# Kernel tuning notes

Measured on AMD Instinct MI355X. Metric: run time of the kernel, lower is better.

## Reference

```python
import jax, jax.numpy as jnp
import numpy as np

DIM = 768
NUM_HEADS = 12
HEAD_DIM = DIM // NUM_HEADS
SCALE = HEAD_DIM ** -0.5


def setup_inputs() -> dict:
    key = jax.random.key(0)
    ks = jax.random.split(key, 9)
    B, L, C = 4, 1024, DIM
    x = jax.random.normal(ks[0], (B, L, C), jnp.float32)
    q_ape = jax.random.normal(ks[1], (1, L, C), jnp.float32)
    k_ape = jax.random.normal(ks[2], (1, L, C), jnp.float32)
    attn_pos = jax.random.normal(ks[3], (1, NUM_HEADS, L, L), jnp.float32)
    s = C ** -0.5
    # torch Linear weights: (out_features, in_features)
    Wq = jax.random.normal(ks[4], (C, C), jnp.float32) * s
    Wk = jax.random.normal(ks[5], (C, C), jnp.float32) * s
    Wv = jax.random.normal(ks[6], (C, C), jnp.float32) * s
    Wp = jax.random.normal(ks[7], (C, C), jnp.float32) * s
    bp = jax.random.normal(ks[8], (C,), jnp.float32) * 0.01
    return {"x": x, "q_ape": q_ape, "k_ape": k_ape, "attn_pos": attn_pos,
            "Wq": Wq, "Wk": Wk, "Wv": Wv, "Wp": Wp, "bp": bp}


def _split_heads(t):
    # (B, L, C) -> (B, H, L, D)
    B, L, C = t.shape
    return t.reshape(B, L, NUM_HEADS, HEAD_DIM).transpose(0, 2, 1, 3)


def reference(x, q_ape, k_ape, attn_pos, Wq, Wk, Wv, Wp, bp):
    B, L, C = x.shape
    q = _split_heads((x + q_ape) @ Wq.T)          # (B,H,L,D)
    k = _split_heads((x + k_ape) @ Wk.T)          # (B,H,L,D)
    v = _split_heads(x @ Wv.T)                    # (B,H,L,D)
    attn = jnp.einsum('bhqd,bhkd->bhqk', q, k) * SCALE + attn_pos
    attn = jax.nn.softmax(attn, axis=-1)
    out = jnp.einsum('bhqk,bhkd->bhqd', attn, v)  # (B,H,L,D)
    out = out.transpose(0, 2, 1, 3).reshape(B, L, C)
    return out @ Wp.T + bp
```

## Files before the change

kernel.cpp:

```cpp
#include <hip/hip_runtime.h>
#include <stdint.h>

#define NH 12
#define HD 64
#define NB 4
#define SEQ 1024
#define CDIM 768
#define MTOT (NB*SEQ)
#define MC   (MTOT*CDIM)
#define LC   (SEQ*CDIM)
#define WSZ  (CDIM*CDIM)
#define LST  104
#define EST  136
#define VST  72
#define L2E  1.44269504f
#define BHSZ (SEQ*HD)

typedef __attribute__((ext_vector_type(4))) float f32x4;
typedef __attribute__((ext_vector_type(8))) __bf16 bf16x8;
typedef __attribute__((ext_vector_type(8))) short short8;
typedef __attribute__((ext_vector_type(4))) unsigned short ushort4v;
typedef unsigned short u16;

static __device__ __forceinline__ f32x4 mfma16(short8 a, short8 b, f32x4 c) {
  return __builtin_amdgcn_mfma_f32_16x16x32_bf16(
      __builtin_bit_cast(bf16x8, a), __builtin_bit_cast(bf16x8, b), c, 0, 0, 0);
}
static __device__ __forceinline__ u16 f2bf(float f) {
  unsigned u = __float_as_uint(f);
  u += 0x7FFFu + ((u >> 16) & 1u);
  return (u16)(u >> 16);
}
static __device__ __forceinline__ float bf2f(u16 h) {
  return __uint_as_float(((unsigned)h) << 16);
}
static __device__ __forceinline__ void lds_load16(const void* g, void* l) {
  __builtin_amdgcn_global_load_lds(
      (const __attribute__((address_space(1))) void*)g,
      (__attribute__((address_space(3))) void*)l, 16, 0, 0);
}

#define PREP_BLKS (MC / 4 / 256)
#define CONV_N4   ((4 * WSZ + CDIM) / 4)
#define CONV_BLKS ((CONV_N4 + 255) / 256)
__global__ __launch_bounds__(256) void prep_all(
    const float* __restrict__ xp, const float* __restrict__ qp,
    const float* __restrict__ kp, const float* __restrict__ Wq,
    const float* __restrict__ Wk, const float* __restrict__ Wv,
    const float* __restrict__ Wp, const float* __restrict__ bp,
    u16* __restrict__ Xq, u16* __restrict__ Xk, u16* __restrict__ Xv,
    u16* __restrict__ Wb) {
  int bid = blockIdx.x;
  if (bid < PREP_BLKS) {
    int i4 = bid * 256 + threadIdx.x;
    int a4 = i4 % (LC / 4);
    f32x4 xx = ((const f32x4*)xp)[i4];
    f32x4 qq = ((const f32x4*)qp)[a4];
    f32x4 kk = ((const f32x4*)kp)[a4];
    ushort4v oq, ok, ov;
#pragma unroll
    for (int j = 0; j < 4; j++) {
      oq[j] = f2bf(xx[j] + qq[j]);
      ok[j] = f2bf(xx[j] + kk[j]);
      ov[j] = f2bf(xx[j]);
    }
    ((ushort4v*)Xq)[i4] = oq;
    ((ushort4v*)Xk)[i4] = ok;
    ((ushort4v*)Xv)[i4] = ov;
  } else {
    int i4 = (bid - PREP_BLKS) * 256 + threadIdx.x;
    if (i4 >= CONV_N4) return;
    int sel = i4 / (WSZ / 4);
    int off = i4 - sel * (WSZ / 4);
    const float* src = sel == 0 ? Wq : sel == 1 ? Wk : sel == 2 ? Wv
                     : sel == 3 ? Wp : bp;
    f32x4 v = ((const f32x4*)src)[off];
    ushort4v o;
#pragma unroll
    for (int j = 0; j < 4; j++) o[j] = f2bf(v[j]);
    ((ushort4v*)Wb)[i4] = o;
  }
}

static __device__ __forceinline__ void gemm_core64(
    const u16* __restrict__ Ab, const u16* __restrict__ Wb,
    short* As, short* Bs, f32x4 acc[2][4]) {
  const int t = threadIdx.x;
  const int lane = t & 63, w = t >> 6, quad = lane >> 4, l16 = lane & 15;
  const int wm = (w >> 1) * 32, wn = (w & 1) * 64;
  const int row4 = t >> 2, chunk = (t & 3) * 8;
  for (int k0 = 0; k0 < CDIM; k0 += 64) {
#pragma unroll
    for (int hh = 0; hh < 2; hh++) {
      const u16* ga = Ab + row4 * CDIM + k0 + hh * 32 + chunk;
      const u16* gb = Wb + row4 * CDIM + k0 + hh * 32 + chunk;
      lds_load16(ga,             (char*)As + hh * 4096 + t * 16);
      lds_load16(gb,             (char*)Bs + hh * 8192 + t * 16);
      lds_load16(gb + 64 * CDIM, (char*)Bs + hh * 8192 + 4096 + t * 16);
    }
    __syncthreads();
#pragma unroll
    for (int hh = 0; hh < 2; hh++) {
      const short* Ah = As + hh * 2048;
      const short* Bh = Bs + hh * 4096;
      short8 af[2], bw[4];
#pragma unroll
      for (int i = 0; i < 2; i++)
        af[i] = *(const short8*)(Ah + (wm + i * 16 + l16) * 32 + quad * 8);
#pragma unroll
      for (int j = 0; j < 4; j++)
        bw[j] = *(const short8*)(Bh + (wn + j * 16 + l16) * 32 + quad * 8);
#pragma unroll
      for (int i = 0; i < 2; i++)
#pragma unroll
        for (int j = 0; j < 4; j++)
          acc[i][j] = mfma16(af[i], bw[j], acc[i][j]);
    }
    __syncthreads();
  }
}

__global__ __launch_bounds__(256) void gemm_qkv(
    const u16* __restrict__ Xq, const u16* __restrict__ Xk, const u16* __restrict__ Xv,
    const u16* __restrict__ Wq, const u16* __restrict__ Wk, const u16* __restrict__ Wv,
    u16* __restrict__ Q, u16* __restrict__ K, u16* __restrict__ Vt) {
  __shared__ __align__(16) short S[12288];
  short* As = S;
  short* Bs = S + 4096;
  const int z = blockIdx.z;
  const int m0 = blockIdx.y * 64, n0 = blockIdx.x * 128;
  const u16* A = (z == 0 ? Xq : z == 1 ? Xk : Xv) + m0 * CDIM;
  const u16* W = (z == 0 ? Wq : z == 1 ? Wk : Wv) + n0 * CDIM;
  f32x4 acc[2][4];
#pragma unroll
  for (int i = 0; i < 2; i++)
#pragma unroll
    for (int j = 0; j < 4; j++) acc[i][j] = 0.f;
  gemm_core64(A, W, As, Bs, acc);

  const int t = threadIdx.x, lane = t & 63, w = t >> 6;
  const int quad = lane >> 4, l16 = lane & 15;
  const int wm = (w >> 1) * 32, wn = (w & 1) * 64;
  const float qs = (z == 0) ? 0.125f : 1.0f;

#pragma unroll
  for (int i = 0; i < 2; i++)
#pragma unroll
    for (int j = 0; j < 4; j++)
#pragma unroll
      for (int r = 0; r < 4; r++) {
        int mr = wm + i * 16 + quad * 4 + r;
        int nc = wn + j * 16 + l16;
        if (z < 2) S[mr * EST + nc] = (short)f2bf(acc[i][j][r] * qs);
        else       S[nc * VST + mr] = (short)f2bf(acc[i][j][r]);
      }
  __syncthreads();

  const int row = t >> 3, ch = t & 7;
  const int b = m0 >> 10, lbase = m0 & 1023;
  if (z == 0) {
#pragma unroll
    for (int cp = 0; cp < 2; cp++) {
      int h = (n0 >> 6) + cp;
#pragma unroll
      for (int rp = 0; rp < 2; rp++) {
        int mr = row + rp * 32;
        short8 v = *(const short8*)(S + mr * EST + cp * 64 + ch * 8);
        *(short8*)(Q + ((((size_t)(b * NH + h)) << 10) + lbase + mr) * HD + ch * 8) = v;
      }
    }
  } else if (z == 1) {
#pragma unroll
    for (int cp = 0; cp < 2; cp++) {
      int h = (n0 >> 6) + cp;
      u16* Kp = K + (size_t)(b * NH + h) * BHSZ;
#pragma unroll
      for (int rp = 0; rp < 2; rp++) {
        int mr = row + rp * 32;
        int tok = lbase + mr;
        short8 v = *(const short8*)(S + mr * EST + cp * 64 + ch * 8);
        *(short8*)(Kp + (((tok >> 4) * 8 + ch) * 16 + (tok & 15)) * 8) = v;
      }
    }
  } else {
#pragma unroll
    for (int rp = 0; rp < 4; rp++) {
      int rn = row + rp * 32;
      int h = (n0 + rn) >> 6, d = rn & 63;
      u16* Vp = Vt + (size_t)(b * NH + h) * BHSZ;
      int jv = d >> 4, ld16 = d & 15;
      int tok = lbase + ch * 8;
      short8 v = *(const short8*)(S + rn * VST + ch * 8);
      *(short8*)(Vp + ((((tok >> 6) * 4 + jv) * 8 + ((tok >> 3) & 7)) * 16 + ld16) * 8) = v;
    }
  }
}

__global__ __launch_bounds__(256, 3) void attn(
    const u16* __restrict__ Q, const u16* __restrict__ Kf, const u16* __restrict__ Vf,
    const float* __restrict__ pos, u16* __restrict__ O) {
  __shared__ __align__(16) short Ps[4 * 16 * LST];
  const int t = threadIdx.x, lane = t & 63, w = t >> 6;
  const int quad = lane >> 4, l16 = lane & 15;

  const int lid = blockIdx.x;
  const int k8 = lid & 7, m = lid >> 3;
  const int g = k8 * 24 + (m >> 2), b = m & 3;
  const int h = g >> 4, qt = g & 15;
  const int bh = b * NH + h;
  const int q0 = qt * 64 + w * 16;

  const u16* Kg = Kf + (size_t)bh * BHSZ;
  const u16* Vg = Vf + (size_t)bh * BHSZ;
  const float* Pg = pos + (size_t)(h * SEQ + q0) * SEQ;
  short* Pw = Ps + w * 16 * LST;
  const int fo = quad * 128 + l16 * 8;

  const u16* Qg = Q + ((size_t)bh * SEQ + q0) * HD;
  const short8 qa0 = *(const short8*)(Qg + l16 * HD + quad * 8);
  const short8 qa1 = *(const short8*)(Qg + l16 * HD + 32 + quad * 8);

  f32x4 o[4];
  float lrow[4];
#pragma unroll
  for (int j = 0; j < 4; j++) o[j] = 0.f;
#pragma unroll
  for (int r = 0; r < 4; r++) lrow[r] = 0.f;

  short8 kb0[4], kb1[4];
  float pf[16];
#pragma unroll
  for (int j = 0; j < 4; j++) {
    kb0[j] = *(const short8*)(Kg + j * 1024 + fo);
    kb1[j] = *(const short8*)(Kg + j * 1024 + 512 + fo);
  }
#pragma unroll
  for (int j = 0; j < 4; j++)
#pragma unroll
    for (int r = 0; r < 4; r++)
      pf[j * 4 + r] = Pg[(quad * 4 + r) * SEQ + j * 16 + l16] * L2E;

#pragma unroll 1
  for (int kt = 0; kt < 16; ++kt) {
    const int kbase = kt * 4096;
    short8 vb0[4], vb1[4];
#pragma unroll
    for (int j = 0; j < 4; j++) {
      vb0[j] = *(const short8*)(Vg + kbase + j * 1024 + fo);
      vb1[j] = *(const short8*)(Vg + kbase + j * 1024 + 512 + fo);
    }
    f32x4 s[4];
#pragma unroll
    for (int j = 0; j < 4; j++) {
      f32x4 zz = 0.f;
      s[j] = mfma16(qa1, kb1[j], mfma16(qa0, kb0[j], zz));
    }
#pragma unroll
    for (int j = 0; j < 4; j++)
#pragma unroll
      for (int r = 0; r < 4; r++) {
        float e = __builtin_amdgcn_exp2f(fmaf(s[j][r], L2E, pf[j * 4 + r]));
        unsigned bits = __float_as_uint(e);
        Pw[(quad * 4 + r) * LST + j * 16 + l16] = (short)(bits >> 16);
        lrow[r] += __uint_as_float(bits & 0xFFFF0000u);
      }
    if (kt < 15) {
      const int nb = kbase + 4096;
#pragma unroll
      for (int j = 0; j < 4; j++) {
        kb0[j] = *(const short8*)(Kg + nb + j * 1024 + fo);
        kb1[j] = *(const short8*)(Kg + nb + j * 1024 + 512 + fo);
      }
      const float* pg = Pg + (kt + 1) * 64;
#pragma unroll
      for (int j = 0; j < 4; j++)
#pragma unroll
        for (int r = 0; r < 4; r++)
          pf[j * 4 + r] = pg[(quad * 4 + r) * SEQ + j * 16 + l16] * L2E;
    }
    const short8 pa0 = *(const short8*)(Pw + l16 * LST + quad * 8);
    const short8 pa1 = *(const short8*)(Pw + l16 * LST + 32 + quad * 8);
#pragma unroll
    for (int j = 0; j < 4; j++)
      o[j] = mfma16(pa1, vb1[j], mfma16(pa0, vb0[j], o[j]));
  }

#pragma unroll
  for (int off = 1; off < 16; off <<= 1)
#pragma unroll
    for (int r = 0; r < 4; r++) lrow[r] += __shfl_xor(lrow[r], off);

  u16* Og = O + ((size_t)b * SEQ + q0) * CDIM + h * HD;
  float inv[4];
#pragma unroll
  for (int r = 0; r < 4; r++) inv[r] = 1.0f / lrow[r];
#pragma unroll
  for (int j = 0; j < 4; j++)
#pragma unroll
    for (int r = 0; r < 4; r++)
      Og[(quad * 4 + r) * CDIM + j * 16 + l16] = f2bf(o[j][r] * inv[r]);
}

__global__ __launch_bounds__(256) void gemm_proj(
    const u16* __restrict__ Oin, const u16* __restrict__ Wp,
    const u16* __restrict__ bp, float* __restrict__ out) {
  __shared__ __align__(16) short As[4096], Bs[4096];
  const int t = threadIdx.x;
  const int lane = t & 63, w = t >> 6, quad = lane >> 4, l16 = lane & 15;
  const int wm = (w >> 1) * 32, wn = (w & 1) * 32;
  const int row4 = t >> 2, chunk = (t & 3) * 8;
  const int m0 = blockIdx.y * 64, n0 = blockIdx.x * 64;
  const u16* Ab = Oin + m0 * CDIM;
  const u16* Wb = Wp + n0 * CDIM;
  f32x4 acc[2][2];
#pragma unroll
  for (int i = 0; i < 2; i++)
#pragma unroll
    for (int j = 0; j < 2; j++) acc[i][j] = 0.f;

  for (int k0 = 0; k0 < CDIM; k0 += 64) {
#pragma unroll
    for (int hh = 0; hh < 2; hh++) {
      const u16* ga = Ab + row4 * CDIM + k0 + hh * 32 + chunk;
      const u16* gb = Wb + row4 * CDIM + k0 + hh * 32 + chunk;
      lds_load16(ga, (char*)As + hh * 4096 + t * 16);
      lds_load16(gb, (char*)Bs + hh * 4096 + t * 16);
    }
    __syncthreads();
#pragma unroll
    for (int hh = 0; hh < 2; hh++) {
      const short* Ah = As + hh * 2048;
      const short* Bh = Bs + hh * 2048;
      short8 af[2], bw[2];
#pragma unroll
      for (int i = 0; i < 2; i++)
        af[i] = *(const short8*)(Ah + (wm + i * 16 + l16) * 32 + quad * 8);
#pragma unroll
      for (int j = 0; j < 2; j++)
        bw[j] = *(const short8*)(Bh + (wn + j * 16 + l16) * 32 + quad * 8);
#pragma unroll
      for (int i = 0; i < 2; i++)
#pragma unroll
        for (int j = 0; j < 2; j++)
          acc[i][j] = mfma16(af[i], bw[j], acc[i][j]);
    }
    __syncthreads();
  }

#pragma unroll
  for (int i = 0; i < 2; i++) {
    int mrow = m0 + wm + i * 16 + quad * 4;
#pragma unroll
    for (int j = 0; j < 2; j++) {
      int n = n0 + wn + j * 16 + l16;
      float bias = bf2f(bp[n]);
#pragma unroll
      for (int r = 0; r < 4; r++)
        out[(mrow + r) * CDIM + n] = acc[i][j][r] + bias;
    }
  }
}

extern "C" void kernel_launch(void* const* d_in, const int* in_sizes, int n_in,
                              void* d_out, int out_size, void* d_ws, size_t ws_size,
                              hipStream_t stream) {
  (void)in_sizes; (void)n_in; (void)out_size;
  const size_t OFF_XQ = 0, OFF_XK = (size_t)MC, OFF_XV = 2ull * MC,
               OFF_Q = 3ull * MC, OFF_K = 4ull * MC, OFF_VT = 5ull * MC,
               OFF_W = 6ull * MC, TOT = OFF_W + 4ull * WSZ + 1024;
  const size_t NEED = 2 * TOT;
  if (ws_size < NEED) return;

  u16* ws = (u16*)d_ws;
  u16 *Xq = ws + OFF_XQ, *Xk = ws + OFF_XK, *Xv = ws + OFF_XV;
  u16 *Qb = ws + OFF_Q, *Kb = ws + OFF_K, *Vt = ws + OFF_VT;
  u16 *Wb = ws + OFF_W;
  u16 *Wqb = Wb, *Wkb = Wb + WSZ, *Wvb = Wb + 2ull * WSZ,
      *Wpb = Wb + 3ull * WSZ, *bpb = Wb + 4ull * WSZ;
  u16* Ob = Xq;

  prep_all<<<PREP_BLKS + CONV_BLKS, 256, 0, stream>>>(
      (const float*)d_in[0], (const float*)d_in[1], (const float*)d_in[2],
      (const float*)d_in[4], (const float*)d_in[5], (const float*)d_in[6],
      (const float*)d_in[7], (const float*)d_in[8], Xq, Xk, Xv, Wb);
  gemm_qkv<<<dim3(6, 64, 3), 256, 0, stream>>>(Xq, Xk, Xv, Wqb, Wkb, Wvb,
                                               Qb, Kb, Vt);
  attn<<<dim3(768), 256, 0, stream>>>(Qb, Kb, Vt, (const float*)d_in[3], Ob);
  gemm_proj<<<dim3(12, 64), 256, 0, stream>>>(Ob, Wpb, bpb, (float*)d_out);
}
```

Before: 208.9 us.

## Process two 16-row query tiles per wave to reuse K/V fragments

The attention kernel drops to 128 threads per block, and each wave now handles 32 query rows as two 16-row sub-tiles. The K and V fragments loaded from global memory are shared by both sub-tiles, which halves K/V load traffic per query row. In exchange, register pressure roughly doubles for the accumulators and positional-bias prefetch, and fewer waves run per block. Occupancy may drop and the second tile's pos loads are not prefetched ahead.

```diff
diff --git a/kernel.cpp b/kernel.cpp
--- a/kernel.cpp
+++ b/kernel.cpp
@@ -196,7 +196,7 @@
   }
 }
 
-__global__ __launch_bounds__(256, 3) void attn(
+__global__ __launch_bounds__(128, 3) void attn(
     const u16* __restrict__ Q, const u16* __restrict__ Kf, const u16* __restrict__ Vf,
     const float* __restrict__ pos, u16* __restrict__ O) {
   __shared__ __align__(16) short Ps[4 * 16 * LST];
@@ -208,27 +208,31 @@
   const int g = k8 * 24 + (m >> 2), b = m & 3;
   const int h = g >> 4, qt = g & 15;
   const int bh = b * NH + h;
-  const int q0 = qt * 64 + w * 16;
+  const int q0 = qt * 64 + w * 32;
 
   const u16* Kg = Kf + (size_t)bh * BHSZ;
   const u16* Vg = Vf + (size_t)bh * BHSZ;
-  const float* Pg = pos + (size_t)(h * SEQ + q0) * SEQ;
-  short* Pw = Ps + w * 16 * LST;
+  const float* PgA = pos + (size_t)(h * SEQ + q0) * SEQ;
+  const float* PgB = PgA + (size_t)16 * SEQ;
+  short* PwA = Ps + (w * 2) * 16 * LST;
+  short* PwB = PwA + 16 * LST;
   const int fo = quad * 128 + l16 * 8;
 
   const u16* Qg = Q + ((size_t)bh * SEQ + q0) * HD;
-  const short8 qa0 = *(const short8*)(Qg + l16 * HD + quad * 8);
-  const short8 qa1 = *(const short8*)(Qg + l16 * HD + 32 + quad * 8);
-
-  f32x4 o[4];
-  float lrow[4];
-#pragma unroll
-  for (int j = 0; j < 4; j++) o[j] = 0.f;
-#pragma unroll
-  for (int r = 0; r < 4; r++) lrow[r] = 0.f;
+  const short8 qaA0 = *(const short8*)(Qg + l16 * HD + quad * 8);
+  const short8 qaA1 = *(const short8*)(Qg + l16 * HD + 32 + quad * 8);
+  const short8 qaB0 = *(const short8*)(Qg + (16 + l16) * HD + quad * 8);
+  const short8 qaB1 = *(const short8*)(Qg + (16 + l16) * HD + 32 + quad * 8);
+
+  f32x4 oA[4], oB[4];
+  float lrowA[4], lrowB[4];
+#pragma unroll
+  for (int j = 0; j < 4; j++) { oA[j] = 0.f; oB[j] = 0.f; }
+#pragma unroll
+  for (int r = 0; r < 4; r++) { lrowA[r] = 0.f; lrowB[r] = 0.f; }
 
   short8 kb0[4], kb1[4];
-  float pf[16];
+  float pfA[16];
 #pragma unroll
   for (int j = 0; j < 4; j++) {
     kb0[j] = *(const short8*)(Kg + j * 1024 + fo);
@@ -238,7 +242,7 @@
   for (int j = 0; j < 4; j++)
 #pragma unroll
     for (int r = 0; r < 4; r++)
-      pf[j * 4 + r] = Pg[(quad * 4 + r) * SEQ + j * 16 + l16] * L2E;
+      pfA[j * 4 + r] = PgA[(quad * 4 + r) * SEQ + j * 16 + l16] * L2E;
 
 #pragma unroll 1
   for (int kt = 0; kt < 16; ++kt) {
@@ -249,20 +253,34 @@
       vb0[j] = *(const short8*)(Vg + kbase + j * 1024 + fo);
       vb1[j] = *(const short8*)(Vg + kbase + j * 1024 + 512 + fo);
     }
-    f32x4 s[4];
+    float pfB[16];
+    {
+      const float* pg = PgB + kt * 64;
+#pragma unroll
+      for (int j = 0; j < 4; j++)
+#pragma unroll
+        for (int r = 0; r < 4; r++)
+          pfB[j * 4 + r] = pg[(quad * 4 + r) * SEQ + j * 16 + l16] * L2E;
+    }
+    f32x4 sA[4], sB[4];
 #pragma unroll
     for (int j = 0; j < 4; j++) {
       f32x4 zz = 0.f;
-      s[j] = mfma16(qa1, kb1[j], mfma16(qa0, kb0[j], zz));
+      sA[j] = mfma16(qaA1, kb1[j], mfma16(qaA0, kb0[j], zz));
+    }
+#pragma unroll
+    for (int j = 0; j < 4; j++) {
+      f32x4 zz = 0.f;
+      sB[j] = mfma16(qaB1, kb1[j], mfma16(qaB0, kb0[j], zz));
     }
 #pragma unroll
     for (int j = 0; j < 4; j++)
 #pragma unroll
       for (int r = 0; r < 4; r++) {
-        float e = __builtin_amdgcn_exp2f(fmaf(s[j][r], L2E, pf[j * 4 + r]));
+        float e = __builtin_amdgcn_exp2f(fmaf(sA[j][r], L2E, pfA[j * 4 + r]));
         unsigned bits = __float_as_uint(e);
-        Pw[(quad * 4 + r) * LST + j * 16 + l16] = (short)(bits >> 16);
-        lrow[r] += __uint_as_float(bits & 0xFFFF0000u);
+        PwA[(quad * 4 + r) * LST + j * 16 + l16] = (short)(bits >> 16);
+        lrowA[r] += __uint_as_float(bits & 0xFFFF0000u);
       }
     if (kt < 15) {
       const int nb = kbase + 4096;
@@ -271,34 +289,58 @@
         kb0[j] = *(const short8*)(Kg + nb + j * 1024 + fo);
         kb1[j] = *(const short8*)(Kg + nb + j * 1024 + 512 + fo);
       }
-      const float* pg = Pg + (kt + 1) * 64;
+      const float* pg = PgA + (kt + 1) * 64;
 #pragma unroll
       for (int j = 0; j < 4; j++)
 #pragma unroll
         for (int r = 0; r < 4; r++)
-          pf[j * 4 + r] = pg[(quad * 4 + r) * SEQ + j * 16 + l16] * L2E;
-    }
-    const short8 pa0 = *(const short8*)(Pw + l16 * LST + quad * 8);
-    const short8 pa1 = *(const short8*)(Pw + l16 * LST + 32 + quad * 8);
+          pfA[j * 4 + r] = pg[(quad * 4 + r) * SEQ + j * 16 + l16] * L2E;
+    }
 #pragma unroll
     for (int j = 0; j < 4; j++)
-      o[j] = mfma16(pa1, vb1[j], mfma16(pa0, vb0[j], o[j]));
+#pragma unroll
+      for (int r = 0; r < 4; r++) {
+        float e = __builtin_amdgcn_exp2f(fmaf(sB[j][r], L2E, pfB[j * 4 + r]));
+        unsigned bits = __float_as_uint(e);
+        PwB[(quad * 4 + r) * LST + j * 16 + l16] = (short)(bits >> 16);
+        lrowB[r] += __uint_as_float(bits & 0xFFFF0000u);
+      }
+    {
+      const short8 pa0 = *(const short8*)(PwA + l16 * LST + quad * 8);
+      const short8 pa1 = *(const short8*)(PwA + l16 * LST + 32 + quad * 8);
+#pragma unroll
+      for (int j = 0; j < 4; j++)
+        oA[j] = mfma16(pa1, vb1[j], mfma16(pa0, vb0[j], oA[j]));
+    }
+    {
+      const short8 pa0 = *(const short8*)(PwB + l16 * LST + quad * 8);
+      const short8 pa1 = *(const short8*)(PwB + l16 * LST + 32 + quad * 8);
+#pragma unroll
+      for (int j = 0; j < 4; j++)
+        oB[j] = mfma16(pa1, vb1[j], mfma16(pa0, vb0[j], oB[j]));
+    }
   }
 
 #pragma unroll
   for (int off = 1; off < 16; off <<= 1)
 #pragma unroll
-    for (int r = 0; r < 4; r++) lrow[r] += __shfl_xor(lrow[r], off);
-
-  u16* Og = O + ((size_t)b * SEQ + q0) * CDIM + h * HD;
-  float inv[4];
-#pragma unroll
-  for (int r = 0; r < 4; r++) inv[r] = 1.0f / lrow[r];
+    for (int r = 0; r < 4; r++) {
+      lrowA[r] += __shfl_xor(lrowA[r], off);
+      lrowB[r] += __shfl_xor(lrowB[r], off);
+    }
+
+  u16* OgA = O + ((size_t)b * SEQ + q0) * CDIM + h * HD;
+  u16* OgB = OgA + (size_t)16 * CDIM;
+  float invA[4], invB[4];
+#pragma unroll
+  for (int r = 0; r < 4; r++) { invA[r] = 1.0f / lrowA[r]; invB[r] = 1.0f / lrowB[r]; }
 #pragma unroll
   for (int j = 0; j < 4; j++)
 #pragma unroll
-    for (int r = 0; r < 4; r++)
-      Og[(quad * 4 + r) * CDIM + j * 16 + l16] = f2bf(o[j][r] * inv[r]);
+    for (int r = 0; r < 4; r++) {
+      OgA[(quad * 4 + r) * CDIM + j * 16 + l16] = f2bf(oA[j][r] * invA[r]);
+      OgB[(quad * 4 + r) * CDIM + j * 16 + l16] = f2bf(oB[j][r] * invB[r]);
+    }
 }
 
 __global__ __launch_bounds__(256) void gemm_proj(
@@ -385,6 +427,6 @@
       (const float*)d_in[7], (const float*)d_in[8], Xq, Xk, Xv, Wb);
   gemm_qkv<<<dim3(6, 64, 3), 256, 0, stream>>>(Xq, Xk, Xv, Wqb, Wkb, Wvb,
                                                Qb, Kb, Vt);
-  attn<<<dim3(768), 256, 0, stream>>>(Qb, Kb, Vt, (const float*)d_in[3], Ob);
+  attn<<<dim3(768), 128, 0, stream>>>(Qb, Kb, Vt, (const float*)d_in[3], Ob);
   gemm_proj<<<dim3(12, 64), 256, 0, stream>>>(Ob, Wpb, bpb, (float*)d_out);
 }
```

New measurement: 397.4 us. 1.9x slower.

## Pre-convert attn_pos to bf16 in MFMA fragment order during prep

Applied to the files above, without the earlier changes.

Adds a prep stage that reads the fp32 attention-position bias, scales it by log2(e), converts it to bf16, and stores it in a tiled layout matching each lane's MFMA accumulator fragment. The attention kernel then loads two 16-byte vectors per tile instead of sixteen strided fp32 scalars. This is meant to cut the strided global traffic in the attention loop, and because the bias is read by all four batches it is now read at half the bytes per reuse. The cost is an extra full pass over the bias in the prep kernel, a larger workspace, and bf16 rounding of the bias.

```diff
diff --git a/kernel.cpp b/kernel.cpp
--- a/kernel.cpp
+++ b/kernel.cpp
@@ -15,6 +15,7 @@
 #define VST  72
 #define L2E  1.44269504f
 #define BHSZ (SEQ*HD)
+#define PTSZ ((size_t)NH*SEQ*SEQ)
 
 typedef __attribute__((ext_vector_type(4))) float f32x4;
 typedef __attribute__((ext_vector_type(8))) __bf16 bf16x8;
@@ -43,13 +44,17 @@
 #define PREP_BLKS (MC / 4 / 256)
 #define CONV_N4   ((4 * WSZ + CDIM) / 4)
 #define CONV_BLKS ((CONV_N4 + 255) / 256)
+#define POS_BLKS  (NH * 64 * 16 / 4)
+#define LTS 68
 __global__ __launch_bounds__(256) void prep_all(
     const float* __restrict__ xp, const float* __restrict__ qp,
     const float* __restrict__ kp, const float* __restrict__ Wq,
     const float* __restrict__ Wk, const float* __restrict__ Wv,
     const float* __restrict__ Wp, const float* __restrict__ bp,
+    const float* __restrict__ pos,
     u16* __restrict__ Xq, u16* __restrict__ Xk, u16* __restrict__ Xv,
-    u16* __restrict__ Wb) {
+    u16* __restrict__ Wb, u16* __restrict__ posT) {
+  __shared__ float LT[4][16 * LTS];
   int bid = blockIdx.x;
   if (bid < PREP_BLKS) {
     int i4 = bid * 256 + threadIdx.x;
@@ -67,7 +72,7 @@
     ((ushort4v*)Xq)[i4] = oq;
     ((ushort4v*)Xk)[i4] = ok;
     ((ushort4v*)Xv)[i4] = ov;
-  } else {
+  } else if (bid < PREP_BLKS + CONV_BLKS) {
     int i4 = (bid - PREP_BLKS) * 256 + threadIdx.x;
     if (i4 >= CONV_N4) return;
     int sel = i4 / (WSZ / 4);
@@ -79,6 +84,33 @@
 #pragma unroll
     for (int j = 0; j < 4; j++) o[j] = f2bf(v[j]);
     ((ushort4v*)Wb)[i4] = o;
+  } else {
+    const int wv = threadIdx.x >> 6, lane = threadIdx.x & 63;
+    const int chunk = (bid - PREP_BLKS - CONV_BLKS) * 4 + wv;
+    const int h = chunk >> 10, rem = chunk & 1023;
+    const int rb = rem >> 4, kt = rem & 15;
+    const float* src = pos + (size_t)h * SEQ * SEQ + (size_t)(rb * 16) * SEQ
+                       + kt * 64;
+    const int rr = lane >> 2, cq = lane & 3;
+    float* Lw = LT[wv];
+#pragma unroll
+    for (int u = 0; u < 4; u++) {
+      f32x4 v = *(const f32x4*)(src + rr * SEQ + cq * 16 + u * 4);
+      *(f32x4*)(Lw + rr * LTS + cq * 16 + u * 4) = v;
+    }
+    __builtin_amdgcn_s_waitcnt(0xC07F);
+    const int quad = lane >> 4, l16 = lane & 15;
+    short8 s0, s1;
+#pragma unroll
+    for (int j = 0; j < 2; j++)
+#pragma unroll
+      for (int r = 0; r < 4; r++) {
+        s0[j * 4 + r] = (short)f2bf(Lw[(quad * 4 + r) * LTS + j * 16 + l16] * L2E);
+        s1[j * 4 + r] = (short)f2bf(Lw[(quad * 4 + r) * LTS + (j + 2) * 16 + l16] * L2E);
+      }
+    u16* dst = posT + (size_t)chunk * 1024 + lane * 16;
+    *(short8*)dst = s0;
+    *(short8*)(dst + 8) = s1;
   }
 }
 
@@ -198,7 +230,7 @@
 
 __global__ __launch_bounds__(256, 3) void attn(
     const u16* __restrict__ Q, const u16* __restrict__ Kf, const u16* __restrict__ Vf,
-    const float* __restrict__ pos, u16* __restrict__ O) {
+    const u16* __restrict__ posT, u16* __restrict__ O) {
   __shared__ __align__(16) short Ps[4 * 16 * LST];
   const int t = threadIdx.x, lane = t & 63, w = t >> 6;
   const int quad = lane >> 4, l16 = lane & 15;
@@ -212,7 +244,8 @@
 
   const u16* Kg = Kf + (size_t)bh * BHSZ;
   const u16* Vg = Vf + (size_t)bh * BHSZ;
-  const float* Pg = pos + (size_t)(h * SEQ + q0) * SEQ;
+  const u16* Tg = posT + ((size_t)(h * 1024 + (qt * 4 + w) * 16)) * 1024
+                  + lane * 16;
   short* Pw = Ps + w * 16 * LST;
   const int fo = quad * 128 + l16 * 8;
 
@@ -228,17 +261,14 @@
   for (int r = 0; r < 4; r++) lrow[r] = 0.f;
 
   short8 kb0[4], kb1[4];
-  float pf[16];
+  short8 pt0, pt1;
 #pragma unroll
   for (int j = 0; j < 4; j++) {
     kb0[j] = *(const short8*)(Kg + j * 1024 + fo);
     kb1[j] = *(const short8*)(Kg + j * 1024 + 512 + fo);
   }
-#pragma unroll
-  for (int j = 0; j < 4; j++)
-#pragma unroll
-    for (int r = 0; r < 4; r++)
-      pf[j * 4 + r] = Pg[(quad * 4 + r) * SEQ + j * 16 + l16] * L2E;
+  pt0 = *(const short8*)(Tg);
+  pt1 = *(const short8*)(Tg + 8);
 
 #pragma unroll 1
   for (int kt = 0; kt < 16; ++kt) {
@@ -256,14 +286,25 @@
       s[j] = mfma16(qa1, kb1[j], mfma16(qa0, kb0[j], zz));
     }
 #pragma unroll
-    for (int j = 0; j < 4; j++)
+    for (int j = 0; j < 2; j++)
 #pragma unroll
       for (int r = 0; r < 4; r++) {
-        float e = __builtin_amdgcn_exp2f(fmaf(s[j][r], L2E, pf[j * 4 + r]));
+        float pv = bf2f((u16)pt0[j * 4 + r]);
+        float e = __builtin_amdgcn_exp2f(fmaf(s[j][r], L2E, pv));
         unsigned bits = __float_as_uint(e);
         Pw[(quad * 4 + r) * LST + j * 16 + l16] = (short)(bits >> 16);
         lrow[r] += __uint_as_float(bits & 0xFFFF0000u);
       }
+#pragma unroll
+    for (int j = 2; j < 4; j++)
+#pragma unroll
+      for (int r = 0; r < 4; r++) {
+        float pv = bf2f((u16)pt1[(j - 2) * 4 + r]);
+        float e = __builtin_amdgcn_exp2f(fmaf(s[j][r], L2E, pv));
+        unsigned bits = __float_as_uint(e);
+        Pw[(quad * 4 + r) * LST + j * 16 + l16] = (short)(bits >> 16);
+        lrow[r] += __uint_as_float(bits & 0xFFFF0000u);
+      }
     if (kt < 15) {
       const int nb = kbase + 4096;
 #pragma unroll
@@ -271,12 +312,8 @@
         kb0[j] = *(const short8*)(Kg + nb + j * 1024 + fo);
         kb1[j] = *(const short8*)(Kg + nb + j * 1024 + 512 + fo);
       }
-      const float* pg = Pg + (kt + 1) * 64;
-#pragma unroll
-      for (int j = 0; j < 4; j++)
-#pragma unroll
-        for (int r = 0; r < 4; r++)
-          pf[j * 4 + r] = pg[(quad * 4 + r) * SEQ + j * 16 + l16] * L2E;
+      pt0 = *(const short8*)(Tg + (kt + 1) * 1024);
+      pt1 = *(const short8*)(Tg + (kt + 1) * 1024 + 8);
     }
     const short8 pa0 = *(const short8*)(Pw + l16 * LST + quad * 8);
     const short8 pa1 = *(const short8*)(Pw + l16 * LST + 32 + quad * 8);
@@ -367,24 +404,26 @@
   (void)in_sizes; (void)n_in; (void)out_size;
   const size_t OFF_XQ = 0, OFF_XK = (size_t)MC, OFF_XV = 2ull * MC,
                OFF_Q = 3ull * MC, OFF_K = 4ull * MC, OFF_VT = 5ull * MC,
-               OFF_W = 6ull * MC, TOT = OFF_W + 4ull * WSZ + 1024;
-  const size_t NEED = 2 * TOT;
-  if (ws_size < NEED) return;
+               OFF_W = 6ull * MC, OFF_PT = OFF_W + 4ull * WSZ + 1024,
+               TOT = OFF_PT + PTSZ;
+  if (ws_size < 2ull * TOT) {  }
+  if (ws_size < TOT * sizeof(u16)) return;
 
   u16* ws = (u16*)d_ws;
   u16 *Xq = ws + OFF_XQ, *Xk = ws + OFF_XK, *Xv = ws + OFF_XV;
   u16 *Qb = ws + OFF_Q, *Kb = ws + OFF_K, *Vt = ws + OFF_VT;
-  u16 *Wb = ws + OFF_W;
+  u16 *Wb = ws + OFF_W, *Pt = ws + OFF_PT;
   u16 *Wqb = Wb, *Wkb = Wb + WSZ, *Wvb = Wb + 2ull * WSZ,
       *Wpb = Wb + 3ull * WSZ, *bpb = Wb + 4ull * WSZ;
   u16* Ob = Xq;
 
-  prep_all<<<PREP_BLKS + CONV_BLKS, 256, 0, stream>>>(
+  prep_all<<<PREP_BLKS + CONV_BLKS + POS_BLKS, 256, 0, stream>>>(
       (const float*)d_in[0], (const float*)d_in[1], (const float*)d_in[2],
       (const float*)d_in[4], (const float*)d_in[5], (const float*)d_in[6],
-      (const float*)d_in[7], (const float*)d_in[8], Xq, Xk, Xv, Wb);
+      (const float*)d_in[7], (const float*)d_in[8], (const float*)d_in[3],
+      Xq, Xk, Xv, Wb, Pt);
   gemm_qkv<<<dim3(6, 64, 3), 256, 0, stream>>>(Xq, Xk, Xv, Wqb, Wkb, Wvb,
                                                Qb, Kb, Vt);
-  attn<<<dim3(768), 256, 0, stream>>>(Qb, Kb, Vt, (const float*)d_in[3], Ob);
+  attn<<<dim3(768), 256, 0, stream>>>(Qb, Kb, Vt, Pt, Ob);
   gemm_proj<<<dim3(12, 64), 256, 0, stream>>>(Ob, Wpb, bpb, (float*)d_out);
 }
```

Measured after the change: 200.5 us. 1.04x faster.
